# Kernel tuning notes

Measured on AMD Instinct MI355X. Metric: run time of the kernel, lower is better.

The kernel has to match this reference:

```python
import jax, jax.numpy as jnp
import numpy as np

B, T, K, H, NH = 16, 2048, 128, 1024, 8
NEG = -jnp.inf


def _ln(x, g, b, eps=1e-5):
    m = x.mean(-1, keepdims=True)
    v = ((x - m) ** 2).mean(-1, keepdims=True)
    return (x - m) * jax.lax.rsqrt(v + eps) * g + b


def _mha(q, k, v, in_w, in_b, out_w, out_b, nh, bias):
    # torch nn.MultiheadAttention (batch_first, eval mode). bias: additive mask (B or 1, 1, Lq, Lk)
    Bq, Lq, Hd = q.shape
    Lk = k.shape[1]
    d = Hd // nh
    wq, wk, wv = in_w[:Hd], in_w[Hd:2 * Hd], in_w[2 * Hd:]
    bq, bk, bv = in_b[:Hd], in_b[Hd:2 * Hd], in_b[2 * Hd:]
    qh = (q @ wq.T + bq).reshape(Bq, Lq, nh, d).transpose(0, 2, 1, 3)
    kh = (k @ wk.T + bk).reshape(Bq, Lk, nh, d).transpose(0, 2, 1, 3)
    vh = (v @ wv.T + bv).reshape(Bq, Lk, nh, d).transpose(0, 2, 1, 3)
    scores = jnp.einsum('bhqd,bhkd->bhqk', qh, kh) * (1.0 / np.sqrt(d)) + bias
    attn = jax.nn.softmax(scores, axis=-1)
    o = jnp.einsum('bhqk,bhkd->bhqd', attn, vh).transpose(0, 2, 1, 3).reshape(Bq, Lq, Hd)
    return o @ out_w.T + out_b


def setup_inputs() -> dict:
    key = jax.random.key(0)
    ks = jax.random.split(key, 12)
    projected = jax.random.normal(ks[0], (B, T, H), dtype=jnp.float32)
    starts = jnp.sort(jax.random.randint(ks[1], (B, K), 0, T - 1), axis=-1)
    widths = jax.random.randint(ks[2], (B, K), 1, 33)
    ends = jnp.minimum(starts + widths, T)
    boundaries = jnp.stack([starts, ends], axis=-1).astype(jnp.int64)
    slot_mask = jnp.ones((B, K), dtype=jnp.float32)
    s = 0.02
    p = {
        'qp_w': jax.random.normal(ks[3], (H, H)) * s, 'qp_b': jnp.zeros((H,)),
        'ca_in_w': jax.random.normal(ks[4], (3 * H, H)) * s, 'ca_in_b': jnp.zeros((3 * H,)),
        'ca_out_w': jax.random.normal(ks[5], (H, H)) * s, 'ca_out_b': jnp.zeros((H,)),
        'cn_g': jnp.ones((H,)), 'cn_b': jnp.zeros((H,)),
        'sa_in_w': jax.random.normal(ks[6], (3 * H, H)) * s, 'sa_in_b': jnp.zeros((3 * H,)),
        'sa_out_w': jax.random.normal(ks[7], (H, H)) * s, 'sa_out_b': jnp.zeros((H,)),
        'on_g': jnp.ones((H,)), 'on_b': jnp.zeros((H,)),
    }
    return {'projected': projected, 'boundaries': boundaries, 'slot_mask': slot_mask, **p}


def reference(projected, boundaries, slot_mask, qp_w, qp_b, ca_in_w, ca_in_b, ca_out_w, ca_out_b,
              cn_g, cn_b, sa_in_w, sa_in_b, sa_out_w, sa_out_b, on_g, on_b):
    Bb, Tt, Hh = projected.shape
    Kk = slot_mask.shape[1]
    tidx = jnp.arange(Tt)
    starts = boundaries[:, :, 0]  # (B,K)
    ends = boundaries[:, :, 1]
    # in-boundary membership: (B,K,T)
    in_bkt = (tidx[None, None, :] >= starts[:, :, None]) & (tidx[None, None, :] < ends[:, :, None])
    valid = slot_mask > 0.5  # (B,K)
    # --- mean-pool init queries ---
    in_slot = (in_bkt & (slot_mask[:, :, None] > 0)).astype(projected.dtype)  # (B,K,T)
    w = in_slot / jnp.clip(in_slot.sum(axis=-1, keepdims=True), 1.0, None)
    init_slots = jnp.einsum('bkt,bth->bkh', w, projected)
    queries = init_slots @ qp_w.T + qp_b
    # --- boundary-masked cross attention (True = blocked) ---
    blocked = ~(in_bkt & valid[:, :, None])  # (B,K,T)
    cross_bias = jnp.where(blocked, NEG, 0.0)[:, None, :, :]  # (B,1,K,T)
    attn_out = _mha(queries, projected, projected, ca_in_w, ca_in_b, ca_out_w, ca_out_b, NH, cross_bias)
    slots = _ln(attn_out + queries, cn_g, cn_b)
    # --- causal self-attention over slots with key padding ---
    causal = jnp.where(jnp.triu(jnp.ones((Kk, Kk), bool), 1), NEG, 0.0)[None, None, :, :]
    pad = jnp.where(slot_mask[:, None, None, :] < 0.5, NEG, 0.0)  # (B,1,1,K)
    ctx = _mha(slots, slots, slots, sa_in_w, sa_in_b, sa_out_w, sa_out_b, NH, causal + pad)
    return _ln(ctx + slots, on_g, on_b)
```

## Files before the change

kernel.cpp:

```cpp
#include <hip/hip_runtime.h>
#include <hip/hip_bf16.h>


#define Bc 16
#define Tc 2048
#define Kc 128
#define Hc 1024
#define NHc 8

typedef unsigned short u16;
typedef __attribute__((ext_vector_type(8))) short short8v;
typedef __attribute__((ext_vector_type(4))) float f32x4;

__device__ __forceinline__ float bf2f(u16 u){ return __uint_as_float(((unsigned)u)<<16); }
__device__ __forceinline__ u16 f2bf(float f){
  unsigned x = __float_as_uint(f);
  return (u16)((x + 0x7fffu + ((x>>16)&1u)) >> 16);
}
__device__ __forceinline__ float4 ld4(const float* p){ return *(const float4*)p; }
__device__ __forceinline__ float ldx(const void* x, size_t idx, bool isbf){
  return isbf ? bf2f(((const u16*)x)[idx]) : ((const float*)x)[idx];
}
__device__ __forceinline__ bool probe_bf(const u16* probe){ return probe[0] == 0x3F80; }

struct CvtArgs { const void* src[15]; int n[15]; long long off[15]; int tobf[15]; };

__global__ __launch_bounds__(256) void convert_params(CvtArgs a, float* fbase,
                                                      u16* bbase, const u16* probe)
{
  bool isbf = probe_bf(probe);
  int g = blockIdx.x*256 + threadIdx.x;
  int stride = gridDim.x*256;
  #pragma unroll 1
  for (int seg=0; seg<15; seg++){
    int n = a.n[seg];
    const void* s = a.src[seg];
    if (a.tobf[seg]){
      u16* d = bbase + a.off[seg];
      if (isbf){ const u16* su=(const u16*)s; for (int i=g;i<n;i+=stride) d[i]=su[i]; }
      else     { const float* sf=(const float*)s; for (int i=g;i<n;i+=stride) d[i]=f2bf(sf[i]); }
    } else {
      float* d = fbase + a.off[seg];
      for (int i=g;i<n;i+=stride) d[i] = ldx(s, i, isbf);
    }
  }
}

__global__ __launch_bounds__(256) void transpose_bf(
    const u16* __restrict__ src, u16* __restrict__ dst, int n)
{
  __shared__ u16 t[32][33];
  int bx = blockIdx.x*32, by = blockIdx.y*32;
  int tx = threadIdx.x & 31, ty = threadIdx.x >> 5;
  #pragma unroll
  for (int i=0;i<32;i+=8)
    t[ty+i][tx] = src[(size_t)(by+ty+i)*n + bx+tx];
  __syncthreads();
  #pragma unroll
  for (int i=0;i<32;i+=8)
    dst[(size_t)(bx+ty+i)*n + by+tx] = t[tx][ty+i];
}

__global__ __launch_bounds__(256) void gemm_mfma(
    const void* __restrict__ Ap, const u16* __restrict__ W,
    const float* __restrict__ bias, void* __restrict__ Cp,
    int M, int N, int Kd, int lda, int ldw, int ldc, float alpha,
    int ZH, long long sAb, long long sAh, long long sWb, long long sWh,
    long long sCb, long long sCh, long long sBh, int ABf, int CBf)
{
  __shared__ u16 As[128*40];
  __shared__ u16 Bs[64*40];
  int z = blockIdx.z, bi = z / ZH, hi = z % ZH;
  const u16*   Ab = (const u16*)Ap  + (size_t)bi*sAb + (size_t)hi*sAh;
  const float* Af = (const float*)Ap+ (size_t)bi*sAb + (size_t)hi*sAh;
  W += (size_t)bi*sWb + (size_t)hi*sWh;
  u16*   Cb = (u16*)Cp   + (size_t)bi*sCb + (size_t)hi*sCh;
  float* Cf = (float*)Cp + (size_t)bi*sCb + (size_t)hi*sCh;
  int tid = threadIdx.x;
  int m0 = blockIdx.y*128, n0 = blockIdx.x*64;
  int wave = tid >> 6, lane = tid & 63;
  int wm = (wave >> 1) * 64, wn = (wave & 1) * 32;
  int r = lane & 15, half = lane >> 4;
  int arow = tid >> 1, ak = (tid & 1) << 4;
  int brow = tid >> 2, bk = (tid & 3) << 3;

  f32x4 acc[4][2] = {};

  for (int k0 = 0; k0 < Kd; k0 += 32){
    short8v va0, va1;
    if (ABf){
      const u16* pa = Ab + (size_t)(m0+arow)*lda + k0 + ak;
      va0 = *(const short8v*)pa;
      va1 = *(const short8v*)(pa+8);
    } else {
      const float* pa = Af + (size_t)(m0+arow)*lda + k0 + ak;
      float4 f0 = ld4(pa), f1 = ld4(pa+4), f2 = ld4(pa+8), f3 = ld4(pa+12);
      va0[0]=(short)f2bf(f0.x); va0[1]=(short)f2bf(f0.y);
      va0[2]=(short)f2bf(f0.z); va0[3]=(short)f2bf(f0.w);
      va0[4]=(short)f2bf(f1.x); va0[5]=(short)f2bf(f1.y);
      va0[6]=(short)f2bf(f1.z); va0[7]=(short)f2bf(f1.w);
      va1[0]=(short)f2bf(f2.x); va1[1]=(short)f2bf(f2.y);
      va1[2]=(short)f2bf(f2.z); va1[3]=(short)f2bf(f2.w);
      va1[4]=(short)f2bf(f3.x); va1[5]=(short)f2bf(f3.y);
      va1[6]=(short)f2bf(f3.z); va1[7]=(short)f2bf(f3.w);
    }
    short8v vb = *(const short8v*)(W + (size_t)(n0+brow)*ldw + k0 + bk);
    *(short8v*)&As[arow*40 + ak]     = va0;
    *(short8v*)&As[arow*40 + ak + 8] = va1;
    *(short8v*)&Bs[brow*40 + bk]     = vb;
    __syncthreads();
    short8v a[4], bf[2];
    #pragma unroll
    for (int mi=0;mi<4;mi++)
      a[mi] = *(const short8v*)&As[(wm+mi*16+r)*40 + half*8];
    #pragma unroll
    for (int ni=0;ni<2;ni++)
      bf[ni] = *(const short8v*)&Bs[(wn+ni*16+r)*40 + half*8];
    #pragma unroll
    for (int mi=0;mi<4;mi++)
      #pragma unroll
      for (int ni=0;ni<2;ni++)
        acc[mi][ni] = __builtin_amdgcn_mfma_f32_16x16x32_bf16(a[mi], bf[ni], acc[mi][ni], 0, 0, 0);
    __syncthreads();
  }

  #pragma unroll
  for (int ni=0;ni<2;ni++){
    int col = n0 + wn + ni*16 + r;
    float bvv = bias ? bias[(size_t)hi*sBh + col] : 0.f;
    #pragma unroll
    for (int mi=0;mi<4;mi++){
      #pragma unroll
      for (int d=0;d<4;d++){
        int rowc = m0 + wm + mi*16 + half*4 + d;
        float o = alpha*acc[mi][ni][d] + bvv;
        if (CBf) Cb[(size_t)rowc*ldc + col] = f2bf(o);
        else     Cf[(size_t)rowc*ldc + col] = o;
      }
    }
  }
}

__global__ __launch_bounds__(256) void gemm_nt(
    const float* __restrict__ A, const float* __restrict__ W,
    const float* __restrict__ bias, float* __restrict__ C,
    int M, int N, int Kd, int lda, int ldw, int ldc, float alpha,
    int ZH, long long sAb, long long sAh, long long sWb, long long sWh,
    long long sCb, long long sCh, long long sBh)
{
  __shared__ float As[16][68];
  __shared__ float Bs[16][68];
  int z = blockIdx.z, bi = z / ZH, hi = z % ZH;
  A += (size_t)bi*sAb + (size_t)hi*sAh;
  W += (size_t)bi*sWb + (size_t)hi*sWh;
  C += (size_t)bi*sCb + (size_t)hi*sCh;
  int tid = threadIdx.x;
  int m0 = blockIdx.y*64, n0 = blockIdx.x*64;
  int tx = tid & 15, ty = tid >> 4;
  int lRow = tid >> 2, lK = (tid & 3) << 2;
  float acc[4][4] = {};
  for (int k0=0; k0<Kd; k0+=16){
    float4 av = ld4(A + (size_t)(m0+lRow)*lda + k0 + lK);
    float4 wv = ld4(W + (size_t)(n0+lRow)*ldw + k0 + lK);
    As[lK+0][lRow]=av.x; As[lK+1][lRow]=av.y; As[lK+2][lRow]=av.z; As[lK+3][lRow]=av.w;
    Bs[lK+0][lRow]=wv.x; Bs[lK+1][lRow]=wv.y; Bs[lK+2][lRow]=wv.z; Bs[lK+3][lRow]=wv.w;
    __syncthreads();
    #pragma unroll
    for (int kk=0;kk<16;kk++){
      float a[4], b[4];
      #pragma unroll
      for (int i=0;i<4;i++) a[i]=As[kk][ty*4+i];
      #pragma unroll
      for (int j=0;j<4;j++) b[j]=Bs[kk][tx*4+j];
      #pragma unroll
      for (int i=0;i<4;i++)
        #pragma unroll
        for (int j=0;j<4;j++)
          acc[i][j] += a[i]*b[j];
    }
    __syncthreads();
  }
  float bv[4] = {0.f,0.f,0.f,0.f};
  if (bias){
    const float* bp = bias + (size_t)hi*sBh + n0 + tx*4;
    bv[0]=bp[0]; bv[1]=bp[1]; bv[2]=bp[2]; bv[3]=bp[3];
  }
  #pragma unroll
  for (int i=0;i<4;i++){
    float4 o;
    o.x = alpha*acc[i][0]+bv[0];
    o.y = alpha*acc[i][1]+bv[1];
    o.z = alpha*acc[i][2]+bv[2];
    o.w = alpha*acc[i][3]+bv[3];
    *(float4*)(C + (size_t)(m0+ty*4+i)*ldc + n0 + tx*4) = o;
  }
}

__global__ __launch_bounds__(256) void gemm_nn(
    const float* __restrict__ A, const float* __restrict__ Bm,
    const float* __restrict__ bias, float* __restrict__ C,
    int M, int N, int Kd, int lda, int ldb, int ldc, float alpha,
    int ZH, long long sAb, long long sAh, long long sBb, long long sBh,
    long long sCb, long long sCh, long long sBiash)
{
  __shared__ float As[16][68];
  __shared__ float Bs[16][68];
  int z = blockIdx.z, bi = z / ZH, hi = z % ZH;
  A  += (size_t)bi*sAb + (size_t)hi*sAh;
  Bm += (size_t)bi*sBb + (size_t)hi*sBh;
  C  += (size_t)bi*sCb + (size_t)hi*sCh;
  int tid = threadIdx.x;
  int m0 = blockIdx.y*64, n0 = blockIdx.x*64;
  int tx = tid & 15, ty = tid >> 4;
  int lRow = tid >> 2, lK = (tid & 3) << 2;
  int bKr = tid >> 4, bNc = (tid & 15) << 2;
  float acc[4][4] = {};
  for (int k0=0; k0<Kd; k0+=16){
    float4 av = ld4(A + (size_t)(m0+lRow)*lda + k0 + lK);
    float4 bvv = ld4(Bm + (size_t)(k0+bKr)*ldb + n0 + bNc);
    As[lK+0][lRow]=av.x; As[lK+1][lRow]=av.y; As[lK+2][lRow]=av.z; As[lK+3][lRow]=av.w;
    *(float4*)&Bs[bKr][bNc] = bvv;
    __syncthreads();
    #pragma unroll
    for (int kk=0;kk<16;kk++){
      float a[4], b[4];
      #pragma unroll
      for (int i=0;i<4;i++) a[i]=As[kk][ty*4+i];
      #pragma unroll
      for (int j=0;j<4;j++) b[j]=Bs[kk][tx*4+j];
      #pragma unroll
      for (int i=0;i<4;i++)
        #pragma unroll
        for (int j=0;j<4;j++)
          acc[i][j] += a[i]*b[j];
    }
    __syncthreads();
  }
  float bv[4] = {0.f,0.f,0.f,0.f};
  if (bias){
    const float* bp = bias + (size_t)hi*sBiash + n0 + tx*4;
    bv[0]=bp[0]; bv[1]=bp[1]; bv[2]=bp[2]; bv[3]=bp[3];
  }
  #pragma unroll
  for (int i=0;i<4;i++){
    float4 o;
    o.x = alpha*acc[i][0]+bv[0];
    o.y = alpha*acc[i][1]+bv[1];
    o.z = alpha*acc[i][2]+bv[2];
    o.w = alpha*acc[i][3]+bv[3];
    *(float4*)(C + (size_t)(m0+ty*4+i)*ldc + n0 + tx*4) = o;
  }
}

__global__ __launch_bounds__(256) void pool_kernel(
    const void* __restrict__ x, const int* __restrict__ bnd,
    const float* __restrict__ maskf, u16* __restrict__ out,
    const u16* __restrict__ probe)
{
  bool isbf = probe_bf(probe);
  bool is64 = (bnd[1] == 0);
  int slot = blockIdx.x; int b = slot >> 7; int tid = threadIdx.x;
  int s0 = is64 ? bnd[4*slot]   : bnd[2*slot];
  int e0 = is64 ? bnd[4*slot+2] : bnd[2*slot+1];
  int d0 = tid*4;
  float acc[4] = {0.f,0.f,0.f,0.f};
  for (int t=s0; t<e0; t++){
    size_t base = ((size_t)b*Tc + (size_t)t)*Hc + d0;
    if (isbf){
      ushort4 v = *(const ushort4*)((const u16*)x + base);
      acc[0]+=bf2f(v.x); acc[1]+=bf2f(v.y); acc[2]+=bf2f(v.z); acc[3]+=bf2f(v.w);
    } else {
      float4 v = ld4((const float*)x + base);
      acc[0]+=v.x; acc[1]+=v.y; acc[2]+=v.z; acc[3]+=v.w;
    }
  }
  int cnt = e0 - s0; if (cnt < 1) cnt = 1;
  float inv = (maskf[slot] > 0.5f) ? 1.f/(float)cnt : 0.f;
  ushort4 o;
  o.x=f2bf(acc[0]*inv); o.y=f2bf(acc[1]*inv); o.z=f2bf(acc[2]*inv); o.w=f2bf(acc[3]*inv);
  *(ushort4*)(out + (size_t)slot*Hc + d0) = o;
}

__global__ __launch_bounds__(512, 2) void cross_attn2(
    const void* __restrict__ x, const int* __restrict__ bnd,
    const u16* __restrict__ Yg, u16* __restrict__ pooled,
    const u16* __restrict__ probe)
{
  __shared__ u16 Xs[32*1024];
  __shared__ float sc[8*32];
  __shared__ float pt[32*8];
  bool isbf = probe_bf(probe);
  bool is64 = (bnd[1] == 0);
  int slot = blockIdx.x; int b = slot >> 7;
  int tid = threadIdx.x;
  int wv = tid >> 6, lane = tid & 63;
  int s0 = is64 ? bnd[4*slot]   : bnd[2*slot];
  int e0 = is64 ? bnd[4*slot+2] : bnd[2*slot+1];
  int w = e0 - s0;

  {
    int rrow = tid >> 7;
    int c = (tid & 127) * 8;
    for (int t = rrow; t < w; t += 4){
      size_t base = ((size_t)b*Tc + (size_t)(s0+t))*Hc + c;
      if (isbf){
        *(short8v*)&Xs[t*1024 + c] = *(const short8v*)((const u16*)x + base);
      } else {
        const float* xf = (const float*)x + base;
        float4 f0 = ld4(xf), f1 = ld4(xf+4);
        short8v v;
        v[0]=(short)f2bf(f0.x); v[1]=(short)f2bf(f0.y);
        v[2]=(short)f2bf(f0.z); v[3]=(short)f2bf(f0.w);
        v[4]=(short)f2bf(f1.x); v[5]=(short)f2bf(f1.y);
        v[6]=(short)f2bf(f1.z); v[7]=(short)f2bf(f1.w);
        *(short8v*)&Xs[t*1024 + c] = v;
      }
    }
  }

  float yf[2][8][8];
  #pragma unroll
  for (int rr=0; rr<2; rr++)
    #pragma unroll
    for (int h=0; h<8; h++){
      short8v yv = *(const short8v*)(Yg + (size_t)slot*8192 + h*1024 + rr*512 + lane*8);
      #pragma unroll
      for (int e=0;e<8;e++) yf[rr][h][e] = bf2f((u16)yv[e]);
    }
  __syncthreads();

  const float scale = 0.08838834764831845f;
  for (int t = wv; t < w; t += 8){
    float acc[8] = {0.f,0.f,0.f,0.f,0.f,0.f,0.f,0.f};
    #pragma unroll
    for (int rr=0; rr<2; rr++){
      short8v xv = *(const short8v*)&Xs[t*1024 + rr*512 + lane*8];
      float xf8[8];
      #pragma unroll
      for (int e=0;e<8;e++) xf8[e] = bf2f((u16)xv[e]);
      #pragma unroll
      for (int h=0;h<8;h++)
        #pragma unroll
        for (int e=0;e<8;e++) acc[h] += yf[rr][h][e]*xf8[e];
    }
    #pragma unroll
    for (int h=0;h<8;h++){
      float v = acc[h];
      for (int off=32; off; off>>=1) v += __shfl_xor(v, off);
      if (lane==0) sc[h*32 + t] = v*scale;
    }
  }
  __syncthreads();

  if (tid < 256){
    int h = tid >> 5, t = tid & 31;
    float v = (t < w) ? sc[h*32 + t] : -1e30f;
    float m = v;
    for (int off=16; off; off>>=1) m = fmaxf(m, __shfl_xor(m, off));
    float e = (t < w) ? __expf(v - m) : 0.f;
    float s = e;
    for (int off=16; off; off>>=1) s += __shfl_xor(s, off);
    pt[t*8 + h] = e / s;
  }
  __syncthreads();

  {
    int d0 = tid*2;
    float pa[8][2] = {};
    for (int t=0; t<w; t++){
      float4 p0 = *(const float4*)&pt[t*8];
      float4 p1 = *(const float4*)&pt[t*8+4];
      unsigned xw = *(const unsigned*)&Xs[t*1024 + d0];
      float x0 = bf2f((u16)(xw & 0xffffu));
      float x1 = bf2f((u16)(xw >> 16));
      pa[0][0]+=p0.x*x0; pa[0][1]+=p0.x*x1;
      pa[1][0]+=p0.y*x0; pa[1][1]+=p0.y*x1;
      pa[2][0]+=p0.z*x0; pa[2][1]+=p0.z*x1;
      pa[3][0]+=p0.w*x0; pa[3][1]+=p0.w*x1;
      pa[4][0]+=p1.x*x0; pa[4][1]+=p1.x*x1;
      pa[5][0]+=p1.y*x0; pa[5][1]+=p1.y*x1;
      pa[6][0]+=p1.z*x0; pa[6][1]+=p1.z*x1;
      pa[7][0]+=p1.w*x0; pa[7][1]+=p1.w*x1;
    }
    #pragma unroll
    for (int h=0;h<8;h++){
      ushort2 o; o.x = f2bf(pa[h][0]); o.y = f2bf(pa[h][1]);
      *(ushort2*)(pooled + (size_t)slot*8192 + h*1024 + d0) = o;
    }
  }
}

__global__ __launch_bounds__(256) void ln_res(
    const float* __restrict__ xin, const float* __restrict__ res,
    const float* __restrict__ g, const float* __restrict__ bb,
    float* __restrict__ outf, u16* __restrict__ outb, const u16* __restrict__ probe)
{
  __shared__ float red[256];
  bool tobf = (probe != nullptr) && probe_bf(probe);
  int row = blockIdx.x, tid = threadIdx.x;
  const float* xr = xin + (size_t)row*1024;
  const float* rr = res + (size_t)row*1024;
  float v[4]; float s = 0.f;
  #pragma unroll
  for (int r=0;r<4;r++){ v[r] = xr[tid+256*r] + rr[tid+256*r]; s += v[r]; }
  red[tid] = s; __syncthreads();
  for (int off=128; off>0; off>>=1){ if (tid<off) red[tid]+=red[tid+off]; __syncthreads(); }
  float mean = red[0] * (1.f/1024.f);
  __syncthreads();
  float s2 = 0.f;
  #pragma unroll
  for (int r=0;r<4;r++){ float d = v[r]-mean; s2 += d*d; }
  red[tid]=s2; __syncthreads();
  for (int off=128; off>0; off>>=1){ if (tid<off) red[tid]+=red[tid+off]; __syncthreads(); }
  float var = red[0]*(1.f/1024.f);
  float rs = rsqrtf(var + 1e-5f);
  #pragma unroll
  for (int r=0;r<4;r++){
    int c = tid+256*r;
    float o = (v[r]-mean)*rs*g[c] + bb[c];
    if (tobf) outb[(size_t)row*1024 + c] = f2bf(o);
    else      outf[(size_t)row*1024 + c] = o;
  }
}

__global__ __launch_bounds__(256) void sa_softmax(float* __restrict__ S,
                                                  const float* __restrict__ maskf)
{
  int wv = threadIdx.x>>6, lane = threadIdx.x&63;
  int row = blockIdx.x*4 + wv;
  int z = row >> 7, q = row & 127;
  int b = z >> 3;
  float* Sr = S + (size_t)row*128;
  float v0 = Sr[lane], v1 = Sr[lane+64];
  if (lane    > q || maskf[b*128+lane   ] < 0.5f) v0 = -1e30f;
  if (lane+64 > q || maskf[b*128+lane+64] < 0.5f) v1 = -1e30f;
  float m = fmaxf(v0,v1);
  for (int off=32; off; off>>=1) m = fmaxf(m, __shfl_xor(m,off));
  float e0 = expf(v0-m), e1 = expf(v1-m);
  float s = e0+e1;
  for (int off=32; off; off>>=1) s += __shfl_xor(s,off);
  float inv = 1.f/s;
  Sr[lane] = e0*inv; Sr[lane+64] = e1*inv;
}

extern "C" void kernel_launch(void* const* d_in, const int* in_sizes, int n_in,
                              void* d_out, int out_size, void* d_ws, size_t ws_size,
                              hipStream_t stream)
{
  const void* x       = d_in[0];
  const int* bnd      = (const int*)d_in[1];
  const u16* probe    = (const u16*)d_in[9];
  float* ws = (float*)d_ws;

  const long long F_qp_b    = 0;
  const long long F_ca_in_b = 1024;
  const long long F_ca_out_b= 4096;
  const long long F_cn_g    = 5120;
  const long long F_cn_b    = 6144;
  const long long F_sa_in_b = 7168;
  const long long F_sa_out_b= 10240;
  const long long F_on_g    = 11264;
  const long long F_on_b    = 12288;
  const long long F_smask   = 13312;
  u16* wb = (u16*)(ws + 15360);
  const long long B_qp_w    = 0;
  const long long B_ca_in_w = 1048576;
  const long long B_ca_out_w= 4194304;
  const long long B_sa_in_w = 5242880;
  const long long B_sa_out_w= 8388608;
  const long long B_wkT     = 9437184;
  const long long PB        = 5258240;

  u16*   islots = (u16*)(ws + PB);
  float* qbuf   = ws + PB + 1048576;
  u16*   qhbuf  = (u16*)(ws + PB + 3145728);
  u16*   Ybuf   = (u16*)(ws + PB + 4194304);
  u16*   poolb  = (u16*)(ws + PB + 12582912);
  u16*   attnb  = (u16*)(ws + PB + 20971520);
  float* attn2  = ws + PB + 22020096;
  float* slots  = ws + PB + 24117248;
  float* qkv    = ws + PB + 26214400;
  float* Sb     = ws + PB + 32505856;
  float* ctx    = ws + PB + 34603008;
  float* ctx2   = ws + PB + 36700160;
  if (ws_size < 44055552ull*4ull) return;

  CvtArgs ca;
  const int srcIdx[15]     = {3,5,7,11,13, 4,6,8,9,10,12,14,15,16, 2};
  const long long offs[15] = {B_qp_w,B_ca_in_w,B_ca_out_w,B_sa_in_w,B_sa_out_w,
                              F_qp_b,F_ca_in_b,F_ca_out_b,F_cn_g,F_cn_b,
                              F_sa_in_b,F_sa_out_b,F_on_g,F_on_b,F_smask};
  const int tobf[15]       = {1,1,1,1,1, 0,0,0,0,0,0,0,0,0, 0};
  for (int i=0;i<15;i++){ ca.src[i]=d_in[srcIdx[i]]; ca.n[i]=in_sizes[srcIdx[i]];
                          ca.off[i]=offs[i]; ca.tobf[i]=tobf[i]; }
  convert_params<<<dim3(4096),dim3(256),0,stream>>>(ca, ws, wb, probe);

  const float* Pf = ws;
  transpose_bf<<<dim3(32,32),dim3(256),0,stream>>>(wb + B_ca_in_w + 1048576ll,
      wb + B_wkT, 1024);
  pool_kernel<<<dim3(2048),dim3(256),0,stream>>>(x, bnd, Pf+F_smask, islots, probe);
  gemm_mfma<<<dim3(16,16,1),dim3(256),0,stream>>>(islots, wb+B_qp_w, Pf+F_qp_b, qbuf,
      2048,1024,1024, 1024,1024,1024, 1.f, 1, 0,0, 0,0, 0,0, 0, 1,0);
  gemm_mfma<<<dim3(16,16,1),dim3(256),0,stream>>>(qbuf, wb+B_ca_in_w, Pf+F_ca_in_b, qhbuf,
      2048,1024,1024, 1024,1024,1024, 1.f, 1, 0,0, 0,0, 0,0, 0, 0,1);
  gemm_mfma<<<dim3(16,16,8),dim3(256),0,stream>>>(qhbuf, wb+B_wkT,
      (const float*)nullptr, Ybuf,
      2048,1024,128, 1024,1024,8192, 1.f, 8, 0,128, 0,128, 0,1024, 0, 1,1);
  cross_attn2<<<dim3(2048),dim3(512),0,stream>>>(x, bnd, Ybuf, poolb, probe);
  gemm_mfma<<<dim3(2,16,8),dim3(256),0,stream>>>(poolb, wb+B_ca_in_w+2097152ll,
      Pf+F_ca_in_b+2048, attnb,
      2048,128,1024, 8192,1024,1024, 1.f, 8, 0,1024, 0,131072, 0,128, 128, 1,1);
  gemm_mfma<<<dim3(16,16,1),dim3(256),0,stream>>>(attnb, wb+B_ca_out_w, Pf+F_ca_out_b, attn2,
      2048,1024,1024, 1024,1024,1024, 1.f, 1, 0,0, 0,0, 0,0, 0, 1,0);
  ln_res<<<dim3(2048),dim3(256),0,stream>>>(attn2, qbuf, Pf+F_cn_g, Pf+F_cn_b,
      slots, (u16*)nullptr, (const u16*)nullptr);
  gemm_mfma<<<dim3(48,16,1),dim3(256),0,stream>>>(slots, wb+B_sa_in_w, Pf+F_sa_in_b, qkv,
      2048,3072,1024, 1024,1024,3072, 1.f, 1, 0,0, 0,0, 0,0, 0, 0,0);
  gemm_nt<<<dim3(2,2,128),dim3(256),0,stream>>>(qkv, qkv + 1024,
      (const float*)nullptr, Sb,
      128,128,128, 3072,3072,128, 0.08838834764831845f, 8,
      393216,128, 393216,128, 131072,16384, 0);
  sa_softmax<<<dim3(4096),dim3(256),0,stream>>>(Sb, Pf+F_smask);
  gemm_nn<<<dim3(2,2,128),dim3(256),0,stream>>>(Sb, qkv + 2048,
      (const float*)nullptr, ctx,
      128,128,128, 128,3072,1024, 1.f, 8,
      131072,16384, 393216,128, 131072,128, 0);
  gemm_mfma<<<dim3(16,16,1),dim3(256),0,stream>>>(ctx, wb+B_sa_out_w, Pf+F_sa_out_b, ctx2,
      2048,1024,1024, 1024,1024,1024, 1.f, 1, 0,0, 0,0, 0,0, 0, 0,0);
  ln_res<<<dim3(2048),dim3(256),0,stream>>>(ctx2, slots, Pf+F_on_g, Pf+F_on_b,
      (float*)d_out, (u16*)d_out, probe);
}
```

Before: 599.5 us.

## Retile MFMA GEMM to 128x128 with direct global-to-LDS loads and bf16-only inputs

```diff
diff --git a/kernel.cpp b/kernel.cpp
--- a/kernel.cpp
+++ b/kernel.cpp
@@ -22,6 +22,12 @@
   return isbf ? bf2f(((const u16*)x)[idx]) : ((const float*)x)[idx];
 }
 __device__ __forceinline__ bool probe_bf(const u16* probe){ return probe[0] == 0x3F80; }
+
+__device__ __forceinline__ void gload_lds16(const u16* g, u16* l){
+  __builtin_amdgcn_global_load_lds(
+      (const __attribute__((address_space(1))) unsigned int*)g,
+      (__attribute__((address_space(3))) unsigned int*)l, 16, 0, 0);
+}
 
 struct CvtArgs { const void* src[15]; int n[15]; long long off[15]; int tobf[15]; };
 
@@ -62,70 +68,54 @@
 }
 
 __global__ __launch_bounds__(256) void gemm_mfma(
-    const void* __restrict__ Ap, const u16* __restrict__ W,
-    const float* __restrict__ bias, void* __restrict__ Cp,
+    const u16* __restrict__ A, const u16* __restrict__ W,
+    const float* __restrict__ bias, float* __restrict__ Cf, u16* __restrict__ Cb,
     int M, int N, int Kd, int lda, int ldw, int ldc, float alpha,
     int ZH, long long sAb, long long sAh, long long sWb, long long sWh,
-    long long sCb, long long sCh, long long sBh, int ABf, int CBf)
-{
-  __shared__ u16 As[128*40];
-  __shared__ u16 Bs[64*40];
+    long long sCb, long long sCh, long long sBh)
+{
+  __shared__ __align__(16) u16 As[128*32];
+  __shared__ __align__(16) u16 Bs[128*32];
   int z = blockIdx.z, bi = z / ZH, hi = z % ZH;
-  const u16*   Ab = (const u16*)Ap  + (size_t)bi*sAb + (size_t)hi*sAh;
-  const float* Af = (const float*)Ap+ (size_t)bi*sAb + (size_t)hi*sAh;
+  A += (size_t)bi*sAb + (size_t)hi*sAh;
   W += (size_t)bi*sWb + (size_t)hi*sWh;
-  u16*   Cb = (u16*)Cp   + (size_t)bi*sCb + (size_t)hi*sCh;
-  float* Cf = (float*)Cp + (size_t)bi*sCb + (size_t)hi*sCh;
   int tid = threadIdx.x;
-  int m0 = blockIdx.y*128, n0 = blockIdx.x*64;
+  int m0 = blockIdx.y*128, n0 = blockIdx.x*128;
   int wave = tid >> 6, lane = tid & 63;
-  int wm = (wave >> 1) * 64, wn = (wave & 1) * 32;
+  int wm = (wave >> 1)*64, wn = (wave & 1)*64;
   int r = lane & 15, half = lane >> 4;
-  int arow = tid >> 1, ak = (tid & 1) << 4;
-  int brow = tid >> 2, bk = (tid & 3) << 3;
-
-  f32x4 acc[4][2] = {};
+  int srow = wave*32 + (lane >> 2);
+  int skc  = (lane & 3) << 3;
+  u16* ldsA = &As[wave*1024];
+  u16* ldsB = &Bs[wave*1024];
+
+  f32x4 acc[4][4] = {};
 
   for (int k0 = 0; k0 < Kd; k0 += 32){
-    short8v va0, va1;
-    if (ABf){
-      const u16* pa = Ab + (size_t)(m0+arow)*lda + k0 + ak;
-      va0 = *(const short8v*)pa;
-      va1 = *(const short8v*)(pa+8);
-    } else {
-      const float* pa = Af + (size_t)(m0+arow)*lda + k0 + ak;
-      float4 f0 = ld4(pa), f1 = ld4(pa+4), f2 = ld4(pa+8), f3 = ld4(pa+12);
-      va0[0]=(short)f2bf(f0.x); va0[1]=(short)f2bf(f0.y);
-      va0[2]=(short)f2bf(f0.z); va0[3]=(short)f2bf(f0.w);
-      va0[4]=(short)f2bf(f1.x); va0[5]=(short)f2bf(f1.y);
-      va0[6]=(short)f2bf(f1.z); va0[7]=(short)f2bf(f1.w);
-      va1[0]=(short)f2bf(f2.x); va1[1]=(short)f2bf(f2.y);
-      va1[2]=(short)f2bf(f2.z); va1[3]=(short)f2bf(f2.w);
-      va1[4]=(short)f2bf(f3.x); va1[5]=(short)f2bf(f3.y);
-      va1[6]=(short)f2bf(f3.z); va1[7]=(short)f2bf(f3.w);
-    }
-    short8v vb = *(const short8v*)(W + (size_t)(n0+brow)*ldw + k0 + bk);
-    *(short8v*)&As[arow*40 + ak]     = va0;
-    *(short8v*)&As[arow*40 + ak + 8] = va1;
-    *(short8v*)&Bs[brow*40 + bk]     = vb;
+    gload_lds16(A + (size_t)(m0+srow   )*lda + k0 + skc, ldsA);
+    gload_lds16(A + (size_t)(m0+srow+16)*lda + k0 + skc, ldsA + 512);
+    gload_lds16(W + (size_t)(n0+srow   )*ldw + k0 + skc, ldsB);
+    gload_lds16(W + (size_t)(n0+srow+16)*ldw + k0 + skc, ldsB + 512);
     __syncthreads();
-    short8v a[4], bf[2];
+    short8v a[4], b[4];
     #pragma unroll
     for (int mi=0;mi<4;mi++)
-      a[mi] = *(const short8v*)&As[(wm+mi*16+r)*40 + half*8];
-    #pragma unroll
-    for (int ni=0;ni<2;ni++)
-      bf[ni] = *(const short8v*)&Bs[(wn+ni*16+r)*40 + half*8];
+      a[mi] = *(const short8v*)&As[(wm+mi*16+r)*32 + half*8];
+    #pragma unroll
+    for (int ni=0;ni<4;ni++)
+      b[ni] = *(const short8v*)&Bs[(wn+ni*16+r)*32 + half*8];
     #pragma unroll
     for (int mi=0;mi<4;mi++)
       #pragma unroll
-      for (int ni=0;ni<2;ni++)
-        acc[mi][ni] = __builtin_amdgcn_mfma_f32_16x16x32_bf16(a[mi], bf[ni], acc[mi][ni], 0, 0, 0);
+      for (int ni=0;ni<4;ni++)
+        acc[mi][ni] = __builtin_amdgcn_mfma_f32_16x16x32_bf16(a[mi], b[ni], acc[mi][ni], 0, 0, 0);
     __syncthreads();
   }
 
-  #pragma unroll
-  for (int ni=0;ni<2;ni++){
+  float* Cfp = Cf ? Cf + (size_t)bi*sCb + (size_t)hi*sCh : nullptr;
+  u16*   Cbp = Cb ? Cb + (size_t)bi*sCb + (size_t)hi*sCh : nullptr;
+  #pragma unroll
+  for (int ni=0;ni<4;ni++){
     int col = n0 + wn + ni*16 + r;
     float bvv = bias ? bias[(size_t)hi*sBh + col] : 0.f;
     #pragma unroll
@@ -134,8 +124,8 @@
       for (int d=0;d<4;d++){
         int rowc = m0 + wm + mi*16 + half*4 + d;
         float o = alpha*acc[mi][ni][d] + bvv;
-        if (CBf) Cb[(size_t)rowc*ldc + col] = f2bf(o);
-        else     Cf[(size_t)rowc*ldc + col] = o;
+        if (Cfp) Cfp[(size_t)rowc*ldc + col] = o;
+        if (Cbp) Cbp[(size_t)rowc*ldc + col] = f2bf(o);
       }
     }
   }
@@ -198,7 +188,7 @@
 
 __global__ __launch_bounds__(256) void gemm_nn(
     const float* __restrict__ A, const float* __restrict__ Bm,
-    const float* __restrict__ bias, float* __restrict__ C,
+    const float* __restrict__ bias, float* __restrict__ C, u16* __restrict__ Cb,
     int M, int N, int Kd, int lda, int ldb, int ldc, float alpha,
     int ZH, long long sAb, long long sAh, long long sBb, long long sBh,
     long long sCb, long long sCh, long long sBiash)
@@ -208,7 +198,6 @@
   int z = blockIdx.z, bi = z / ZH, hi = z % ZH;
   A  += (size_t)bi*sAb + (size_t)hi*sAh;
   Bm += (size_t)bi*sBb + (size_t)hi*sBh;
-  C  += (size_t)bi*sCb + (size_t)hi*sCh;
   int tid = threadIdx.x;
   int m0 = blockIdx.y*64, n0 = blockIdx.x*64;
   int tx = tid & 15, ty = tid >> 4;
@@ -243,12 +232,20 @@
   }
   #pragma unroll
   for (int i=0;i<4;i++){
-    float4 o;
-    o.x = alpha*acc[i][0]+bv[0];
-    o.y = alpha*acc[i][1]+bv[1];
-    o.z = alpha*acc[i][2]+bv[2];
-    o.w = alpha*acc[i][3]+bv[3];
-    *(float4*)(C + (size_t)(m0+ty*4+i)*ldc + n0 + tx*4) = o;
+    float o0 = alpha*acc[i][0]+bv[0];
+    float o1 = alpha*acc[i][1]+bv[1];
+    float o2 = alpha*acc[i][2]+bv[2];
+    float o3 = alpha*acc[i][3]+bv[3];
+    size_t rowoff = (size_t)(m0+ty*4+i)*ldc + n0 + tx*4;
+    if (Cb){
+      u16* cp = Cb + (size_t)bi*sCb + (size_t)hi*sCh + rowoff;
+      ushort4 ov; ov.x=f2bf(o0); ov.y=f2bf(o1); ov.z=f2bf(o2); ov.w=f2bf(o3);
+      *(ushort4*)cp = ov;
+    } else {
+      float* cp = C + (size_t)bi*sCb + (size_t)hi*sCh + rowoff;
+      float4 ov; ov.x=o0; ov.y=o1; ov.z=o2; ov.w=o3;
+      *(float4*)cp = ov;
+    }
   }
 }
 
@@ -281,14 +278,14 @@
   *(ushort4*)(out + (size_t)slot*Hc + d0) = o;
 }
 
-__global__ __launch_bounds__(512, 2) void cross_attn2(
+__global__ __launch_bounds__(512, 2) void cross_attn3(
     const void* __restrict__ x, const int* __restrict__ bnd,
     const u16* __restrict__ Yg, u16* __restrict__ pooled,
     const u16* __restrict__ probe)
 {
-  __shared__ u16 Xs[32*1024];
+  __shared__ __align__(16) u16 Xs[32*1024];
   __shared__ float sc[8*32];
-  __shared__ float pt[32*8];
+  __shared__ __align__(16) float pt[32*8];
   bool isbf = probe_bf(probe);
   bool is64 = (bnd[1] == 0);
   int slot = blockIdx.x; int b = slot >> 7;
@@ -318,49 +315,38 @@
     }
   }
 
-  float yf[2][8][8];
-  #pragma unroll
-  for (int rr=0; rr<2; rr++)
-    #pragma unroll
-    for (int h=0; h<8; h++){
-      short8v yv = *(const short8v*)(Yg + (size_t)slot*8192 + h*1024 + rr*512 + lane*8);
-      #pragma unroll
-      for (int e=0;e<8;e++) yf[rr][h][e] = bf2f((u16)yv[e]);
-    }
+  int h = wv;
+  float y0[8], y1[8];
+  #pragma unroll
+  for (int r=0;r<8;r++){
+    unsigned yw = *(const unsigned*)(Yg + (size_t)slot*8192 + h*1024 + lane*2 + 128*r);
+    y0[r] = bf2f((u16)(yw & 0xffffu));
+    y1[r] = bf2f((u16)(yw >> 16));
+  }
   __syncthreads();
 
   const float scale = 0.08838834764831845f;
-  for (int t = wv; t < w; t += 8){
-    float acc[8] = {0.f,0.f,0.f,0.f,0.f,0.f,0.f,0.f};
-    #pragma unroll
-    for (int rr=0; rr<2; rr++){
-      short8v xv = *(const short8v*)&Xs[t*1024 + rr*512 + lane*8];
-      float xf8[8];
-      #pragma unroll
-      for (int e=0;e<8;e++) xf8[e] = bf2f((u16)xv[e]);
-      #pragma unroll
-      for (int h=0;h<8;h++)
-        #pragma unroll
-        for (int e=0;e<8;e++) acc[h] += yf[rr][h][e]*xf8[e];
-    }
-    #pragma unroll
-    for (int h=0;h<8;h++){
-      float v = acc[h];
-      for (int off=32; off; off>>=1) v += __shfl_xor(v, off);
-      if (lane==0) sc[h*32 + t] = v*scale;
-    }
+  for (int t=0; t<w; t++){
+    float acc = 0.f;
+    #pragma unroll
+    for (int r=0;r<8;r++){
+      unsigned xw = *(const unsigned*)&Xs[t*1024 + lane*2 + 128*r];
+      acc += y0[r]*bf2f((u16)(xw & 0xffffu)) + y1[r]*bf2f((u16)(xw >> 16));
+    }
+    for (int off=32; off; off>>=1) acc += __shfl_xor(acc, off);
+    if (lane==0) sc[h*32 + t] = acc*scale;
   }
   __syncthreads();
 
   if (tid < 256){
-    int h = tid >> 5, t = tid & 31;
-    float v = (t < w) ? sc[h*32 + t] : -1e30f;
+    int hh = tid >> 5, t = tid & 31;
+    float v = (t < w) ? sc[hh*32 + t] : -1e30f;
     float m = v;
     for (int off=16; off; off>>=1) m = fmaxf(m, __shfl_xor(m, off));
     float e = (t < w) ? __expf(v - m) : 0.f;
     float s = e;
     for (int off=16; off; off>>=1) s += __shfl_xor(s, off);
-    pt[t*8 + h] = e / s;
+    pt[t*8 + hh] = e / s;
   }
   __syncthreads();
 
@@ -383,9 +369,9 @@
       pa[7][0]+=p1.w*x0; pa[7][1]+=p1.w*x1;
     }
     #pragma unroll
-    for (int h=0;h<8;h++){
-      ushort2 o; o.x = f2bf(pa[h][0]); o.y = f2bf(pa[h][1]);
-      *(ushort2*)(pooled + (size_t)slot*8192 + h*1024 + d0) = o;
+    for (int hh=0;hh<8;hh++){
+      ushort2 o; o.x = f2bf(pa[hh][0]); o.y = f2bf(pa[hh][1]);
+      *(ushort2*)(pooled + (size_t)slot*8192 + hh*1024 + d0) = o;
     }
   }
 }
@@ -393,7 +379,8 @@
 __global__ __launch_bounds__(256) void ln_res(
     const float* __restrict__ xin, const float* __restrict__ res,
     const float* __restrict__ g, const float* __restrict__ bb,
-    float* __restrict__ outf, u16* __restrict__ outb, const u16* __restrict__ probe)
+    float* __restrict__ outf, u16* __restrict__ outb, const u16* __restrict__ probe,
+    u16* __restrict__ dualb)
 {
   __shared__ float red[256];
   bool tobf = (probe != nullptr) && probe_bf(probe);
@@ -420,6 +407,7 @@
     float o = (v[r]-mean)*rs*g[c] + bb[c];
     if (tobf) outb[(size_t)row*1024 + c] = f2bf(o);
     else      outf[(size_t)row*1024 + c] = o;
+    if (dualb) dualb[(size_t)row*1024 + c] = f2bf(o);
   }
 }
 
@@ -471,19 +459,21 @@
   const long long B_wkT     = 9437184;
   const long long PB        = 5258240;
 
-  u16*   islots = (u16*)(ws + PB);
-  float* qbuf   = ws + PB + 1048576;
-  u16*   qhbuf  = (u16*)(ws + PB + 3145728);
-  u16*   Ybuf   = (u16*)(ws + PB + 4194304);
-  u16*   poolb  = (u16*)(ws + PB + 12582912);
-  u16*   attnb  = (u16*)(ws + PB + 20971520);
-  float* attn2  = ws + PB + 22020096;
-  float* slots  = ws + PB + 24117248;
-  float* qkv    = ws + PB + 26214400;
-  float* Sb     = ws + PB + 32505856;
-  float* ctx    = ws + PB + 34603008;
-  float* ctx2   = ws + PB + 36700160;
-  if (ws_size < 44055552ull*4ull) return;
+  float* qbuf    = ws + PB + 0;
+  float* slots   = ws + PB + 2097152;
+  u16*   Ybuf    = (u16*)(ws + PB + 4194304);
+  u16*   poolb   = Ybuf;
+  u16*   islots  = (u16*)(ws + PB + 12582912);
+  u16*   qbuf_b  = (u16*)(ws + PB + 13631488);
+  u16*   qhbuf   = (u16*)(ws + PB + 14680064);
+  u16*   attnb   = (u16*)(ws + PB + 15728640);
+  float* attn2   = ws + PB + 16777216;
+  u16*   slots_b = (u16*)(ws + PB + 18874368);
+  float* qkv     = ws + PB + 19922944;
+  float* Sb      = ws + PB + 26214400;
+  u16*   ctx_b   = (u16*)(ws + PB + 28311552);
+  float* ctx2    = ws + PB + 29360128;
+  if (ws_size < (size_t)(PB + 31457280ll) * 4ull) return;
 
   CvtArgs ca;
   const int srcIdx[15]     = {3,5,7,11,13, 4,6,8,9,10,12,14,15,16, 2};
@@ -499,34 +489,39 @@
   transpose_bf<<<dim3(32,32),dim3(256),0,stream>>>(wb + B_ca_in_w + 1048576ll,
       wb + B_wkT, 1024);
   pool_kernel<<<dim3(2048),dim3(256),0,stream>>>(x, bnd, Pf+F_smask, islots, probe);
-  gemm_mfma<<<dim3(16,16,1),dim3(256),0,stream>>>(islots, wb+B_qp_w, Pf+F_qp_b, qbuf,
-      2048,1024,1024, 1024,1024,1024, 1.f, 1, 0,0, 0,0, 0,0, 0, 1,0);
-  gemm_mfma<<<dim3(16,16,1),dim3(256),0,stream>>>(qbuf, wb+B_ca_in_w, Pf+F_ca_in_b, qhbuf,
-      2048,1024,1024, 1024,1024,1024, 1.f, 1, 0,0, 0,0, 0,0, 0, 0,1);
-  gemm_mfma<<<dim3(16,16,8),dim3(256),0,stream>>>(qhbuf, wb+B_wkT,
-      (const float*)nullptr, Ybuf,
-      2048,1024,128, 1024,1024,8192, 1.f, 8, 0,128, 0,128, 0,1024, 0, 1,1);
-  cross_attn2<<<dim3(2048),dim3(512),0,stream>>>(x, bnd, Ybuf, poolb, probe);
-  gemm_mfma<<<dim3(2,16,8),dim3(256),0,stream>>>(poolb, wb+B_ca_in_w+2097152ll,
-      Pf+F_ca_in_b+2048, attnb,
-      2048,128,1024, 8192,1024,1024, 1.f, 8, 0,1024, 0,131072, 0,128, 128, 1,1);
-  gemm_mfma<<<dim3(16,16,1),dim3(256),0,stream>>>(attnb, wb+B_ca_out_w, Pf+F_ca_out_b, attn2,
-      2048,1024,1024, 1024,1024,1024, 1.f, 1, 0,0, 0,0, 0,0, 0, 1,0);
+  gemm_mfma<<<dim3(8,16,1),dim3(256),0,stream>>>(islots, wb+B_qp_w, Pf+F_qp_b,
+      qbuf, qbuf_b,
+      2048,1024,1024, 1024,1024,1024, 1.f, 1, 0,0, 0,0, 0,0, 0);
+  gemm_mfma<<<dim3(8,16,1),dim3(256),0,stream>>>(qbuf_b, wb+B_ca_in_w, Pf+F_ca_in_b,
+      (float*)nullptr, qhbuf,
+      2048,1024,1024, 1024,1024,1024, 1.f, 1, 0,0, 0,0, 0,0, 0);
+  gemm_mfma<<<dim3(8,16,8),dim3(256),0,stream>>>(qhbuf, wb+B_wkT,
+      (const float*)nullptr, (float*)nullptr, Ybuf,
+      2048,1024,128, 1024,1024,8192, 1.f, 8, 0,128, 0,128, 0,1024, 0);
+  cross_attn3<<<dim3(2048),dim3(512),0,stream>>>(x, bnd, Ybuf, poolb, probe);
+  gemm_mfma<<<dim3(1,16,8),dim3(256),0,stream>>>(poolb, wb+B_ca_in_w+2097152ll,
+      Pf+F_ca_in_b+2048, (float*)nullptr, attnb,
+      2048,128,1024, 8192,1024,1024, 1.f, 8, 0,1024, 0,131072, 0,128, 128);
+  gemm_mfma<<<dim3(8,16,1),dim3(256),0,stream>>>(attnb, wb+B_ca_out_w, Pf+F_ca_out_b,
+      attn2, (u16*)nullptr,
+      2048,1024,1024, 1024,1024,1024, 1.f, 1, 0,0, 0,0, 0,0, 0);
   ln_res<<<dim3(2048),dim3(256),0,stream>>>(attn2, qbuf, Pf+F_cn_g, Pf+F_cn_b,
-      slots, (u16*)nullptr, (const u16*)nullptr);
-  gemm_mfma<<<dim3(48,16,1),dim3(256),0,stream>>>(slots, wb+B_sa_in_w, Pf+F_sa_in_b, qkv,
-      2048,3072,1024, 1024,1024,3072, 1.f, 1, 0,0, 0,0, 0,0, 0, 0,0);
+      slots, (u16*)nullptr, (const u16*)nullptr, slots_b);
+  gemm_mfma<<<dim3(24,16,1),dim3(256),0,stream>>>(slots_b, wb+B_sa_in_w, Pf+F_sa_in_b,
+      qkv, (u16*)nullptr,
+      2048,3072,1024, 1024,1024,3072, 1.f, 1, 0,0, 0,0, 0,0, 0);
   gemm_nt<<<dim3(2,2,128),dim3(256),0,stream>>>(qkv, qkv + 1024,
       (const float*)nullptr, Sb,
       128,128,128, 3072,3072,128, 0.08838834764831845f, 8,
       393216,128, 393216,128, 131072,16384, 0);
   sa_softmax<<<dim3(4096),dim3(256),0,stream>>>(Sb, Pf+F_smask);
   gemm_nn<<<dim3(2,2,128),dim3(256),0,stream>>>(Sb, qkv + 2048,
-      (const float*)nullptr, ctx,
+      (const float*)nullptr, (float*)nullptr, ctx_b,
       128,128,128, 128,3072,1024, 1.f, 8,
       131072,16384, 393216,128, 131072,128, 0);
-  gemm_mfma<<<dim3(16,16,1),dim3(256),0,stream>>>(ctx, wb+B_sa_out_w, Pf+F_sa_out_b, ctx2,
-      2048,1024,1024, 1024,1024,1024, 1.f, 1, 0,0, 0,0, 0,0, 0, 0,0);
+  gemm_mfma<<<dim3(8,16,1),dim3(256),0,stream>>>(ctx_b, wb+B_sa_out_w, Pf+F_sa_out_b,
+      ctx2, (u16*)nullptr,
+      2048,1024,1024, 1024,1024,1024, 1.f, 1, 0,0, 0,0, 0,0, 0);
   ln_res<<<dim3(2048),dim3(256),0,stream>>>(ctx2, slots, Pf+F_on_g, Pf+F_on_b,
-      (float*)d_out, (u16*)d_out, probe);
-}
+      (float*)d_out, (u16*)d_out, probe, (u16*)nullptr);
+}
```

Result: faster. 567.7 us (-5.3%).
